# Performance work log

Hardware: AMD Instinct MI355X
Metric: run time of the kernel (lower is better)

The kernel has to match this reference:

```python
import jax, jax.numpy as jnp
import numpy as np

H, W = 512, 512          # resized_height, resized_width
R = 2                    # cdist norm order
B, NGT = 4, 64
MAX_DIST = float(np.sqrt(H ** 2 + W ** 2))
EPS = 1e-6


def setup_inputs() -> dict:
    key = jax.random.key(0)
    k1, k2, k3, k4 = jax.random.split(key, 4)
    prob_map = jax.random.uniform(k1, (B, H, W), dtype=jnp.float32)
    # all entries > 0.2 so the torch filter prob_y[prob_y>0.2] keeps every point
    prob_y = 0.2 + 0.79 * jax.random.uniform(k2, (B, NGT), dtype=jnp.float32)
    gt = jax.random.uniform(k3, (B, NGT, 2), dtype=jnp.float32) * jnp.array([H - 1, W - 1], jnp.float32)
    orig_sizes = jax.random.randint(k4, (B, 2), 512, 2048, dtype=jnp.int32)
    return {"prob_map": prob_map, "prob_y": prob_y, "gt": gt, "orig_sizes": orig_sizes}


def _pixel_locations():
    # cartesian([arange(H), arange(W)]) -> (H*W, 2), row-major
    ii, jj = jnp.meshgrid(jnp.arange(H), jnp.arange(W), indexing="ij")
    return jnp.stack([ii, jj], axis=-1).reshape(-1, 2).astype(jnp.float32)


def _ghd(prob_map, prob_y, gt, orig_sizes):
    locs = _pixel_locations()                      # (P, 2), P = H*W
    resized = jnp.array([H, W], jnp.float32)

    def per_batch(pm, py, g, osz):
        nf = osz.astype(jnp.float32) / resized     # (2,) norm factor
        nx = nf * locs                             # (P, 2)
        ny = nf * g                                # (G, 2)
        diff = jnp.abs(nx[:, None, :] - ny[None, :, :])   # (P, G, 2)
        d = jnp.sum(diff ** R, axis=-1) ** (1.0 / R)      # (P, G)
        p = pm.reshape(-1)                         # (P,)
        n_est_pts = jnp.sum(p)
        n_gt_sum = jnp.sum(jnp.where(py > 0.2, py, 0.0))
        weighted = p[:, None] * py[None, :] * d    # p_x * p_y * d
        term_1 = jnp.sum(jnp.min(weighted, axis=1)) / (n_est_pts + EPS)
        dense = (1.0 - p[:, None]) * MAX_DIST + weighted
        term_2 = jnp.sum(jnp.min(dense, axis=0)) / (n_gt_sum + EPS)
        return term_1, term_2

    t1, t2 = jax.vmap(per_batch)(prob_map, prob_y, gt, orig_sizes)
    return t1.mean() + t2.mean()


def reference(prob_map, prob_y, gt, orig_sizes):
    return _ghd(prob_map, prob_y, gt, orig_sizes)
```

## Files before the change

### kernel.cpp

```cpp
#include <hip/hip_runtime.h>
#include <math.h>

#define HH 512
#define WW 512
#define PP (HH * WW)
#define GG 64
#define BB 4
#define THREADS 512
#define TILE 1024
#define NT (PP / TILE)
#define MAX_DIST 724.0773439350246f
#define EPSV 1e-6f
#define BIGF 3.4e38f


__device__ __forceinline__ float rdlane(float v, int l) {
    return __int_as_float(__builtin_amdgcn_readlane(__float_as_int(v), l));
}

__launch_bounds__(THREADS, 8)
__global__ void ghd_main(const float* __restrict__ prob_map,
                         const float* __restrict__ prob_y,
                         const float* __restrict__ gt,
                         const int*   __restrict__ osz,
                         float*       __restrict__ ws) {
    const int t    = blockIdx.x;
    const int b    = blockIdx.y;
    const int tid  = threadIdx.x;
    const int lane = tid & 63;
    const int wave = tid >> 6;

    __shared__ float wmin[8][GG];
    __shared__ float s_t1[8], s_ne[8];

    const float nf0 = (float)osz[2 * b]     * (1.0f / HH);
    const float nf1 = (float)osz[2 * b + 1] * (1.0f / WW);

    const float2 gxy = ((const float2*)gt)[b * GG + lane];
    const float  gx  = nf0 * gxy.x;
    const float  gy  = nf1 * gxy.y;
    const float  py  = prob_y[b * GG + lane];

    const int    seg0 = t * TILE + wave * 128;
    const float2 p2   = ((const float2*)(prob_map + (size_t)b * PP + seg0))[lane];
    const int    pid0 = seg0 + 2 * lane;
    const float  nx0  = nf0 * (float)(pid0 >> 9);
    const float  nx1a = nf1 * (float)(pid0 & (WW - 1));

    const float* __restrict__ gtb = gt     + (size_t)b * GG * 2;
    const float* __restrict__ pyb = prob_y + (size_t)b * GG;

    float ma = BIGF, mb = BIGF;
#pragma unroll
    for (int g = 0; g < GG; ++g) {
        float sgx = gtb[2 * g];
        float sgy = gtb[2 * g + 1];
        float spy = pyb[g];
        float dx  = fmaf(-nf0, sgx, nx0);
        float dx2 = dx * dx;
        float da  = fmaf(-nf1, sgy, nx1a);
        float db  = da + nf1;
        float pq  = spy * spy;
        ma = fminf(ma, pq * fmaf(da, da, dx2));
        mb = fminf(mb, pq * fmaf(db, db, dx2));
    }
    float t1 = p2.x * __builtin_amdgcn_sqrtf(ma) + p2.y * __builtin_amdgcn_sqrtf(mb);
    float ne = p2.x + p2.y;

    const float dxw  = nf0 * (float)(seg0 >> 9) - gx;
    const float dx2w = dxw * dxw;
    const float negM = -MAX_DIST;
    const float posM =  MAX_DIST;
    float dya  = nf1 * (float)(seg0 & (WW - 1)) - gy;
    float dyb  = dya + nf1;
    const float step = nf1 + nf1;
    float gm0 = BIGF, gm1 = BIGF;
#pragma unroll
    for (int k = 0; k < 64; ++k) {
        float qa  = rdlane(p2.x, k);
        float qb  = rdlane(p2.y, k);
        float ea  = __builtin_amdgcn_sqrtf(fmaf(dya, dya, dx2w));
        float eb  = __builtin_amdgcn_sqrtf(fmaf(dyb, dyb, dx2w));
        gm0 = fminf(gm0, fmaf(qa, fmaf(py, ea, negM), posM));
        gm1 = fminf(gm1, fmaf(qb, fmaf(py, eb, negM), posM));
        dya += step;
        dyb += step;
    }
    wmin[wave][lane] = fminf(gm0, gm1);

#pragma unroll
    for (int off = 1; off < 64; off <<= 1) {
        t1 += __shfl_xor(t1, off);
        ne += __shfl_xor(ne, off);
    }
    if (lane == 0) { s_t1[wave] = t1; s_ne[wave] = ne; }
    __syncthreads();

    if (tid == 0) {
        float st = 0.0f, sn = 0.0f;
#pragma unroll
        for (int w = 0; w < 8; ++w) { st += s_t1[w]; sn += s_ne[w]; }
        ws[256  + b * NT + t] = st;
        ws[1280 + b * NT + t] = sn;
    }
    if (tid < GG) {
        float v = wmin[0][tid];
#pragma unroll
        for (int w = 1; w < 8; ++w) v = fminf(v, wmin[w][tid]);
        atomicMin(reinterpret_cast<unsigned*>(ws) + b * GG + tid, __float_as_uint(v));
    }
}

__global__ void ghd_final(const float* __restrict__ prob_y,
                          const float* __restrict__ ws,
                          float*       __restrict__ out) {
    const int tid = threadIdx.x;
    const int b = tid >> 6;
    const int g = tid & 63;

    float mv  = __uint_as_float(reinterpret_cast<const unsigned*>(ws)[b * GG + g]);
    float py  = prob_y[b * GG + g];
    float pyf = (py > 0.2f) ? py : 0.0f;

    float4 tv = ((const float4*)(ws + 256))[b * (NT / 4) + g];
    float4 nv = ((const float4*)(ws + 1280))[b * (NT / 4) + g];
    float t1s = tv.x + tv.y + tv.z + tv.w;
    float nes = nv.x + nv.y + nv.z + nv.w;

#pragma unroll
    for (int off = 1; off < 64; off <<= 1) {
        mv  += __shfl_xor(mv, off);
        pyf += __shfl_xor(pyf, off);
        t1s += __shfl_xor(t1s, off);
        nes += __shfl_xor(nes, off);
    }
    __shared__ float res[4];
    if (g == 0) res[b] = t1s / (nes + EPSV) + mv / (pyf + EPSV);
    __syncthreads();
    if (tid == 0) out[0] = 0.25f * (res[0] + res[1] + res[2] + res[3]);
}

extern "C" void kernel_launch(void* const* d_in, const int* in_sizes, int n_in,
                              void* d_out, int out_size, void* d_ws, size_t ws_size,
                              hipStream_t stream) {
    const float* prob_map = (const float*)d_in[0];
    const float* prob_y   = (const float*)d_in[1];
    const float* gt       = (const float*)d_in[2];
    const int*   osz      = (const int*)d_in[3];
    float* out = (float*)d_out;
    float* ws  = (float*)d_ws;

    hipMemsetAsync(ws, 0x7f, BB * GG * sizeof(unsigned), stream);

    dim3 grid(NT, BB);
    ghd_main<<<grid, THREADS, 0, stream>>>(prob_map, prob_y, gt, osz, ws);
    ghd_final<<<1, 256, 0, stream>>>(prob_y, ws, out);
}
```

Baseline: 83.88 us.

## Prune ground-truth candidates per wave segment using distance bounds for term_1 min

Each wave covers 128 pixels in one row, so every ground-truth point gets a lower and an upper bound on its weighted squared distance over that segment. Points whose lower bound exceeds the smallest upper bound across the wave are dropped through a ballot mask. The term_1 min loop then visits only the surviving candidates and reads their coordinates with readlane instead of scalar loads. This adds a 6-step shuffle reduction and a data-dependent loop with scalar bit iteration.

```diff
diff --git a/kernel.cpp b/kernel.cpp
--- a/kernel.cpp
+++ b/kernel.cpp
@@ -40,6 +40,7 @@
     const float  gx  = nf0 * gxy.x;
     const float  gy  = nf1 * gxy.y;
     const float  py  = prob_y[b * GG + lane];
+    const float  pyq = py * py;
 
     const int    seg0 = t * TILE + wave * 128;
     const float2 p2   = ((const float2*)(prob_map + (size_t)b * PP + seg0))[lane];
@@ -47,31 +48,43 @@
     const float  nx0  = nf0 * (float)(pid0 >> 9);
     const float  nx1a = nf1 * (float)(pid0 & (WW - 1));
 
-    const float* __restrict__ gtb = gt     + (size_t)b * GG * 2;
-    const float* __restrict__ pyb = prob_y + (size_t)b * GG;
+    const float dxw  = nf0 * (float)(seg0 >> 9) - gx;
+    const float dx2w = dxw * dxw;
+
+    const float c0  = nf1 * (float)(seg0 & (WW - 1));
+    const float cL  = c0 - gy;
+    const float cR  = (c0 + 127.0f * nf1) - gy;
+    const float dmn = fmaxf(fmaxf(cL, -cR), 0.0f);
+    const float dmx = fmaxf(cR, -cL);
+    const float vmin = pyq * fmaf(dmn, dmn, dx2w);
+    const float vmax = pyq * fmaf(dmx, dmx, dx2w);
+    float thr = vmax;
+#pragma unroll
+    for (int off = 1; off < 64; off <<= 1)
+        thr = fminf(thr, __shfl_xor(thr, off));
+    const unsigned long long cand = __ballot(vmin <= thr);
 
     float ma = BIGF, mb = BIGF;
-#pragma unroll
-    for (int g = 0; g < GG; ++g) {
-        float sgx = gtb[2 * g];
-        float sgy = gtb[2 * g + 1];
-        float spy = pyb[g];
-        float dx  = fmaf(-nf0, sgx, nx0);
+    unsigned long long m = cand;
+    while (m) {
+        const int g = (int)__ffsll(m) - 1;
+        m &= m - 1;
+        float sgx = rdlane(gx,  g);
+        float sgy = rdlane(gy,  g);
+        float spq = rdlane(pyq, g);
+        float dx  = nx0 - sgx;
         float dx2 = dx * dx;
-        float da  = fmaf(-nf1, sgy, nx1a);
+        float da  = nx1a - sgy;
         float db  = da + nf1;
-        float pq  = spy * spy;
-        ma = fminf(ma, pq * fmaf(da, da, dx2));
-        mb = fminf(mb, pq * fmaf(db, db, dx2));
+        ma = fminf(ma, spq * fmaf(da, da, dx2));
+        mb = fminf(mb, spq * fmaf(db, db, dx2));
     }
     float t1 = p2.x * __builtin_amdgcn_sqrtf(ma) + p2.y * __builtin_amdgcn_sqrtf(mb);
     float ne = p2.x + p2.y;
 
-    const float dxw  = nf0 * (float)(seg0 >> 9) - gx;
-    const float dx2w = dxw * dxw;
     const float negM = -MAX_DIST;
     const float posM =  MAX_DIST;
-    float dya  = nf1 * (float)(seg0 & (WW - 1)) - gy;
+    float dya  = c0 - gy;
     float dyb  = dya + nf1;
     const float step = nf1 + nf1;
     float gm0 = BIGF, gm1 = BIGF;
```

Result: no change. 82.94 us (-1.1%).
